# Performance work log

Hardware: AMD Instinct MI355X
Metric: run time of the kernel (lower is better)

Reference implementation:

```python
import jax, jax.numpy as jnp
import numpy as np

UP = 2


def _lpf_rect(N, cutoff):
    # ideal lowpass rect over full-FFT frequency axis (with Nyquist 0.5 fix)
    cutoff_low = int((N * cutoff) // 2)
    cutoff_high = int(N - cutoff_low)
    rect = np.ones(N, dtype=np.float32)
    rect[cutoff_low + 1:cutoff_high] = 0.0
    if (N * cutoff) % 2 == 0:
        rect[cutoff_low] = 0.5
        rect[cutoff_high] = 0.5
    return rect


def _recon_rect(N, cutoff):
    # reconstruction rect for zero-insertion upsampling (no Nyquist halving)
    cutoff_low = int((N * cutoff) // 2)
    cutoff_high = int(N - cutoff_low)
    rect = np.ones(N, dtype=np.float32)
    rect[cutoff_low + 1:cutoff_high] = 0.0
    return rect


def _rfft2_mask(rect_h, rect_w):
    # outer product mask on rfft2 grid: full H axis x half W axis
    half_w = rect_w.shape[0] // 2 + 1
    return jnp.asarray(rect_h[:, None] * rect_w[None, :half_w])


def setup_inputs() -> dict:
    key = jax.random.key(0)
    x = jax.random.normal(key, (32, 128, 64, 64), dtype=jnp.float32)
    # PolyAct default init_coef (buffer, non-trainable)
    coef = jnp.array([0.0169394634313126, 0.5, 0.3078363963999393, 0.0],
                     dtype=jnp.float32)
    return {"x": x, "coef": coef}


def reference(x, coef):
    B, C, H, W = x.shape
    Hu, Wu = H * UP, W * UP

    # ---- UpsampleRFFT: zero-insertion then ideal reconstruction filter ----
    xu = jnp.zeros((B, C, Hu, Wu), x.dtype).at[:, :, ::UP, ::UP].set(x)
    recon_mask = _rfft2_mask(_recon_rect(Hu, 1.0 / UP), _recon_rect(Wu, 1.0 / UP))
    f = jnp.fft.rfft2(xu) * (UP * UP) * recon_mask
    xu = jnp.fft.irfft2(f, s=(Hu, Wu))

    # ---- PolyAct: calc_polynomial loops range(2, deg) with deg=3, so only
    # terms up to x^2 are used (coef[3] is never applied) ----
    y = coef[0] + coef[1] * xu + coef[2] * xu * xu

    # ---- LPF_RFFT with cutoff = 1/up ----
    lpf_mask = _rfft2_mask(_lpf_rect(Hu, 1.0 / UP), _lpf_rect(Wu, 1.0 / UP))
    y = jnp.fft.irfft2(jnp.fft.rfft2(y) * lpf_mask, s=(Hu, Wu))

    # ---- decimate back to original resolution ----
    return y[:, :, ::UP, ::UP]
```

## Files before the change

### kernel.cpp

```cpp
#include <hip/hip_runtime.h>
#include <math.h>


typedef short short8 __attribute__((ext_vector_type(8)));
typedef float f32x16 __attribute__((ext_vector_type(16)));

#define LSH 68
#define GSTR 132

__device__ __forceinline__ short f2bf(float f) {
  unsigned u = __float_as_uint(f);
  u += 0x7FFFu + ((u >> 16) & 1u);
  return (short)(u >> 16);
}
__device__ __forceinline__ unsigned pkbf(float a, float b) {
  unsigned ua = __float_as_uint(a); ua += 0x7FFFu + ((ua >> 16) & 1u);
  unsigned ub = __float_as_uint(b); ub += 0x7FFFu + ((ub >> 16) & 1u);
  return (ua >> 16) | (ub & 0xFFFF0000u);
}
__device__ __forceinline__ float bflo(unsigned u) {
  return __uint_as_float(u << 16);
}
__device__ __forceinline__ float bfhi(unsigned u) {
  return __uint_as_float(u & 0xFFFF0000u);
}
__device__ __forceinline__ short8 ldrow(const short* p) {
  union { unsigned u[4]; short8 s; } v;
  const uint2 lo = *(const uint2*)p;
  const uint2 hi = *(const uint2*)(p + 4);
  v.u[0] = lo.x; v.u[1] = lo.y; v.u[2] = hi.x; v.u[3] = hi.y;
  return v.s;
}
__device__ __forceinline__ short8 tabfrag(const short* gtab, int t, int blk,
                                          int kk, int q, int l31) {
  const int s = 64 + 16 * kk + 8 * q - l31 - 32 * blk;
  const int p = s & 3;
  return ldrow(gtab + (t * 4 + p) * GSTR + (s - p));
}

__global__ void init_tables(float* ws) {
  __shared__ float g64s[64];
  const int tid = threadIdx.x;
  if (tid < 64) {
    const int d = 2 * tid + 1;
    double s = 1.0;
    for (int k = 1; k <= 32; ++k) {
      const int qq = (k * d) & 127;
      s += 2.0 * cos(M_PI * (double)qq / 64.0);
    }
    g64s[tid] = (float)(s / 64.0);
  }
  __syncthreads();
  if (tid < 128) ws[tid] = g64s[tid & 63];
  short* gt = (short*)(ws + 128);
  for (int e = tid; e < 2 * 4 * GSTR; e += 256) {
    const int t = e / (4 * GSTR);
    const int rem = e - t * 4 * GSTR;
    const int p = rem / GSTR;
    const int m = rem - p * GSTR;
    const int li = m + p;
    const int gi = t ? ((-li) & 63) : (li & 63);
    gt[e] = f2bf(g64s[gi]);
  }
}

__global__ __launch_bounds__(256, 5) void uppolyact_kernel(
    const float* __restrict__ x, const float* __restrict__ coef,
    const float* __restrict__ ws, float* __restrict__ out) {
  __shared__ __align__(16) short bufA[64 * LSH];
  __shared__ __align__(16) short bufB[64 * LSH];
  __shared__ __align__(16) short bufC[64 * LSH];
  __shared__ __align__(16) unsigned char tabs[2624];
  __shared__ float tp[256];
  __shared__ float up[256];
  __shared__ float tvec[64], uvec[64], svec[64];
  __shared__ float lrp[128];
  __shared__ float sigv;

  const float* g2f = (const float*)tabs;
  const short* gtab = (const short*)(tabs + 512);

  const int tid = threadIdx.x;
  const int lane = tid & 63;
  const int w = tid >> 6;
  const int q = lane >> 5;
  const int l31 = lane & 31;
  const int rb = w >> 1, cb = w & 1;
  const int icol = cb * 32 + l31;
  const size_t base = (size_t)blockIdx.x * 4096;

  if (tid < 164) *(float4*)&tabs[16 * tid] = ((const float4*)ws)[tid];
  {
    const float4* xv = (const float4*)(x + base);
#pragma unroll
    for (int e = 0; e < 4; ++e) {
      const int k4 = tid + 256 * e;
      const float4 v = xv[k4];
      const int r = k4 >> 4, c = (k4 & 15) << 2;
      const unsigned d0 = pkbf(v.x, v.y), d1 = pkbf(v.z, v.w);
      *(uint2*)&bufA[r * LSH + c] = make_uint2(d0, d1);
      bufB[(c + 0) * LSH + r] = (short)d0;
      bufB[(c + 1) * LSH + r] = (short)(d0 >> 16);
      bufB[(c + 2) * LSH + r] = (short)d1;
      bufB[(c + 3) * LSH + r] = (short)(d1 >> 16);
    }
  }
  __syncthreads();

  f32x16 Rt, Lt;
#pragma unroll
  for (int r = 0; r < 16; ++r) { Rt[r] = 0.0f; Lt[r] = 0.0f; }
#pragma unroll
  for (int kk = 0; kk < 4; ++kk) {
    const short8 aR = tabfrag(gtab, 1, rb, kk, q, l31);
    const short8 bR = ldrow(&bufA[(cb * 32 + l31) * LSH + kk * 16 + q * 8]);
    Rt = __builtin_amdgcn_mfma_f32_32x32x16_bf16(aR, bR, Rt, 0, 0, 0);
    const short8 aL = ldrow(&bufB[(rb * 32 + l31) * LSH + kk * 16 + q * 8]);
    const short8 bL = tabfrag(gtab, 1, cb, kk, q, l31);
    Lt = __builtin_amdgcn_mfma_f32_32x32x16_bf16(aL, bL, Lt, 0, 0, 0);
  }
  {
    const int jj = tid & 63, pp = tid >> 6;
    float tacc = 0.0f, uacc = 0.0f;
#pragma unroll
    for (int g4 = 0; g4 < 4; ++g4) {
      const uint2 dt = *(const uint2*)&bufB[jj * LSH + 16 * pp + 4 * g4];
      tacc += bflo(dt.x) - bfhi(dt.x) + bflo(dt.y) - bfhi(dt.y);
      const uint2 du = *(const uint2*)&bufA[jj * LSH + 16 * pp + 4 * g4];
      uacc += bflo(du.x) - bfhi(du.x) + bflo(du.y) - bfhi(du.y);
    }
    tp[pp * 64 + jj] = tacc;
    up[pp * 64 + jj] = uacc;
  }
  {
    float lp = 0.0f;
#pragma unroll
    for (int r = 0; r < 16; ++r) lp += (r & 1) ? -Lt[r] : Lt[r];
    lp += __shfl_xor(lp, 32);
    if (q == 0) lrp[rb * 64 + icol] = lp;
  }
  __syncthreads();

#pragma unroll
  for (int grp = 0; grp < 4; ++grp) {
    const unsigned d0 = pkbf(Lt[4 * grp + 0], Lt[4 * grp + 1]);
    const unsigned d1 = pkbf(Lt[4 * grp + 2], Lt[4 * grp + 3]);
    *(uint2*)&bufC[icol * LSH + 4 * q + 32 * rb + 8 * grp] = make_uint2(d0, d1);
  }
  if (tid < 64) {
    tvec[tid] = tp[tid] + tp[64 + tid] + tp[128 + tid] + tp[192 + tid];
  } else if (tid < 128) {
    const int i = tid - 64;
    uvec[i] = up[i] + up[64 + i] + up[128 + i] + up[192 + i];
  }
  __syncthreads();

  f32x16 OOt;
#pragma unroll
  for (int r = 0; r < 16; ++r) OOt[r] = 0.0f;
#pragma unroll
  for (int kk = 0; kk < 4; ++kk) {
    const short8 a = tabfrag(gtab, 1, rb, kk, q, l31);
    const short8 b = ldrow(&bufC[(cb * 32 + l31) * LSH + kk * 16 + q * 8]);
    OOt = __builtin_amdgcn_mfma_f32_32x32x16_bf16(a, b, OOt, 0, 0, 0);
  }
  {
    const int jj = tid & 63, pp = tid >> 6;
    float sp = 0.0f;
#pragma unroll
    for (int mm = 0; mm < 16; ++mm) {
      const int m = 16 * pp + mm;
      sp += tvec[m] * g2f[64 + jj - m];
    }
    tp[pp * 64 + jj] = sp;
  }
  if (tid >= 192) {
    const int i = tid - 192;
    float v = (i & 1) ? -uvec[i] : uvec[i];
#pragma unroll
    for (int off = 32; off >= 1; off >>= 1) v += __shfl_xor(v, off);
    if (i == 0) sigv = v;
  }
#pragma unroll
  for (int grp = 0; grp < 4; ++grp) {
    const unsigned d0 = pkbf(OOt[4 * grp + 0] * OOt[4 * grp + 0],
                             OOt[4 * grp + 1] * OOt[4 * grp + 1]);
    const unsigned d1 = pkbf(OOt[4 * grp + 2] * OOt[4 * grp + 2],
                             OOt[4 * grp + 3] * OOt[4 * grp + 3]);
    *(uint2*)&bufA[icol * LSH + 4 * q + 32 * rb + 8 * grp] = make_uint2(d0, d1);
  }
  __syncthreads();

  if (tid < 64) {
    svec[tid] = tp[tid] + tp[64 + tid] + tp[128 + tid] + tp[192 + tid];
  }
  __syncthreads();

  const float sgi = (icol & 1) ? -1.0f : 1.0f;
  const float luv_i = lrp[icol] + lrp[64 + icol];
  f32x16 Ut;
#pragma unroll
  for (int grp = 0; grp < 4; ++grp) {
    const float4 sv = *(const float4*)&svec[4 * q + 32 * rb + 8 * grp];
    float zeo[4];
#pragma unroll
    for (int rr = 0; rr < 4; ++rr) {
      const int r = 4 * grp + rr;
      const float veo = Rt[r] + sgi * (&sv.x)[rr] * (1.0f / 64.0f);
      zeo[rr] = veo * veo;
      const float sgj = (r & 1) ? -1.0f : 1.0f;
      const float voe = Lt[r] + luv_i * sgj * (1.0f / 64.0f);
      Ut[r] = voe * voe;
    }
    *(uint2*)&bufB[icol * LSH + 4 * q + 32 * rb + 8 * grp] =
        make_uint2(pkbf(zeo[0], zeo[1]), pkbf(zeo[2], zeo[3]));
  }
#pragma unroll
  for (int kk = 0; kk < 4; ++kk) {
    const short8 aU = tabfrag(gtab, 0, rb, kk, q, l31);
    const short8 bU = ldrow(&bufA[(cb * 32 + l31) * LSH + kk * 16 + q * 8]);
    Ut = __builtin_amdgcn_mfma_f32_32x32x16_bf16(aU, bU, Ut, 0, 0, 0);
  }
#pragma unroll
  for (int r = 0; r < 16; ++r) {
    const int jrow = (r & 3) + 4 * q + 8 * (r >> 2) + 32 * rb;
    bufC[jrow * LSH + icol] = f2bf(Ut[r]);
  }
  __syncthreads();

  f32x16 Wv, Vv;
#pragma unroll
  for (int r = 0; r < 16; ++r) { Wv[r] = 0.0f; Vv[r] = 0.0f; }
#pragma unroll
  for (int kk = 0; kk < 4; ++kk) {
    const short8 aW = ldrow(&bufB[(rb * 32 + l31) * LSH + kk * 16 + q * 8]);
    const short8 bW = tabfrag(gtab, 0, cb, kk, q, l31);
    Wv = __builtin_amdgcn_mfma_f32_32x32x16_bf16(aW, bW, Wv, 0, 0, 0);
    const short8 aV = tabfrag(gtab, 0, rb, kk, q, l31);
    const short8 bV = ldrow(&bufC[(cb * 32 + l31) * LSH + kk * 16 + q * 8]);
    Vv = __builtin_amdgcn_mfma_f32_32x32x16_bf16(aV, bV, Vv, 0, 0, 0);
  }

  const float c0 = coef[0], c1 = coef[1];
  const float c2q = 0.25f * coef[2];
  const float* xb = x + base;
  float* ob = out + base;
  const int jcol = icol;
  const float sgjc = (jcol & 1) ? -1.0f : 1.0f;
  const float tj = tvec[jcol];
#pragma unroll
  for (int grp = 0; grp < 4; ++grp) {
    const float4 uv = *(const float4*)&uvec[4 * q + 32 * rb + 8 * grp];
#pragma unroll
    for (int rr = 0; rr < 4; ++rr) {
      const int r = 4 * grp + rr;
      const int irow = (r & 3) + 4 * q + 8 * (r >> 2) + 32 * rb;
      const float sgir = (r & 1) ? -1.0f : 1.0f;
      const float xg = xb[irow * 64 + jcol];
      const float vee = xg + (sgir * tj + (&uv.x)[rr] * sgjc) * (1.0f / 64.0f) +
                        sgir * sgjc * sigv * (1.0f / 4096.0f);
      ob[irow * 64 + jcol] = c0 + c1 * xg + c2q * (vee * vee + Vv[r] + Wv[r]);
    }
  }
}

extern "C" void kernel_launch(void* const* d_in, const int* in_sizes, int n_in,
                              void* d_out, int out_size, void* d_ws,
                              size_t ws_size, hipStream_t stream) {
  const float* x = (const float*)d_in[0];
  const float* coef = (const float*)d_in[1];
  float* out = (float*)d_out;
  float* ws = (float*)d_ws;
  const int channels = out_size / 4096;
  init_tables<<<dim3(1), dim3(256), 0, stream>>>(ws);
  uppolyact_kernel<<<dim3(channels), dim3(256), 0, stream>>>(x, coef, ws, out);
}
```

Before: 152.1 us.

## Swizzle transposed LDS tile, reuse LDS x, stage coalesced nontemporal output stores

XOR-swizzles the transposed bf16 copy of the input in shared memory to reduce bank conflicts on its row reads. It swaps the roles of bufA and bufB so one barrier and the svec reduction step can be removed, with the partial sums now added inline. The final x values are read from the bf16 shared-memory tile instead of being re-read from global memory. Results are staged through shared memory so the output can be written with coalesced float4 nontemporal stores. Reading x as bf16 lowers the precision of the linear term, and the staging step adds two barriers.

```diff
diff --git a/kernel.cpp b/kernel.cpp
--- a/kernel.cpp
+++ b/kernel.cpp
@@ -4,9 +4,11 @@
 
 typedef short short8 __attribute__((ext_vector_type(8)));
 typedef float f32x16 __attribute__((ext_vector_type(16)));
+typedef float f32x4 __attribute__((ext_vector_type(4)));
 
 #define LSH 68
-#define GSTR 132
+#define GSTR 136
+#define FSTR 68
 
 __device__ __forceinline__ short f2bf(float f) {
   unsigned u = __float_as_uint(f);
@@ -24,12 +26,17 @@
 __device__ __forceinline__ float bfhi(unsigned u) {
   return __uint_as_float(u & 0xFFFF0000u);
 }
-__device__ __forceinline__ short8 ldrow(const short* p) {
+__device__ __forceinline__ short8 mk8(uint2 lo, uint2 hi) {
   union { unsigned u[4]; short8 s; } v;
-  const uint2 lo = *(const uint2*)p;
-  const uint2 hi = *(const uint2*)(p + 4);
   v.u[0] = lo.x; v.u[1] = lo.y; v.u[2] = hi.x; v.u[3] = hi.y;
   return v.s;
+}
+__device__ __forceinline__ short8 ldrow(const short* p) {
+  return mk8(*(const uint2*)p, *(const uint2*)(p + 4));
+}
+__device__ __forceinline__ short8 ldrow_sw(const short* rowp, int u0, int sw) {
+  return mk8(*(const uint2*)(rowp + 4 * (u0 ^ sw)),
+             *(const uint2*)(rowp + 4 * ((u0 + 1) ^ sw)));
 }
 __device__ __forceinline__ short8 tabfrag(const short* gtab, int t, int blk,
                                           int kk, int q, int l31) {
@@ -67,13 +74,15 @@
 __global__ __launch_bounds__(256, 5) void uppolyact_kernel(
     const float* __restrict__ x, const float* __restrict__ coef,
     const float* __restrict__ ws, float* __restrict__ out) {
-  __shared__ __align__(16) short bufA[64 * LSH];
-  __shared__ __align__(16) short bufB[64 * LSH];
-  __shared__ __align__(16) short bufC[64 * LSH];
-  __shared__ __align__(16) unsigned char tabs[2624];
+  __shared__ __align__(16) unsigned char arena[3 * 64 * LSH * 2];
+  short* bufA = (short*)arena;
+  short* bufB = (short*)(arena + 64 * LSH * 2);
+  short* bufC = (short*)(arena + 2 * 64 * LSH * 2);
+  float* fOut = (float*)(arena + 64 * LSH * 2);
+  __shared__ __align__(16) unsigned char tabs[2688];
   __shared__ float tp[256];
   __shared__ float up[256];
-  __shared__ float tvec[64], uvec[64], svec[64];
+  __shared__ float tvec[64], uvec[64];
   __shared__ float lrp[128];
   __shared__ float sigv;
 
@@ -89,20 +98,21 @@
   const int icol = cb * 32 + l31;
   const size_t base = (size_t)blockIdx.x * 4096;
 
-  if (tid < 164) *(float4*)&tabs[16 * tid] = ((const float4*)ws)[tid];
+  if (tid < 168) *(float4*)&tabs[16 * tid] = ((const float4*)ws)[tid];
   {
     const float4* xv = (const float4*)(x + base);
 #pragma unroll
     for (int e = 0; e < 4; ++e) {
       const int k4 = tid + 256 * e;
       const float4 v = xv[k4];
-      const int r = k4 >> 4, c = (k4 & 15) << 2;
+      const int r = k4 >> 4, c4 = k4 & 15, c = c4 << 2;
       const unsigned d0 = pkbf(v.x, v.y), d1 = pkbf(v.z, v.w);
       *(uint2*)&bufA[r * LSH + c] = make_uint2(d0, d1);
-      bufB[(c + 0) * LSH + r] = (short)d0;
-      bufB[(c + 1) * LSH + r] = (short)(d0 >> 16);
-      bufB[(c + 2) * LSH + r] = (short)d1;
-      bufB[(c + 3) * LSH + r] = (short)(d1 >> 16);
+      const int so = 4 * ((r >> 2) ^ c4) + (r & 3);
+      bufB[(c + 0) * LSH + so] = (short)d0;
+      bufB[(c + 1) * LSH + so] = (short)(d0 >> 16);
+      bufB[(c + 2) * LSH + so] = (short)d1;
+      bufB[(c + 3) * LSH + so] = (short)(d1 >> 16);
     }
   }
   __syncthreads();
@@ -110,21 +120,27 @@
   f32x16 Rt, Lt;
 #pragma unroll
   for (int r = 0; r < 16; ++r) { Rt[r] = 0.0f; Lt[r] = 0.0f; }
-#pragma unroll
-  for (int kk = 0; kk < 4; ++kk) {
-    const short8 aR = tabfrag(gtab, 1, rb, kk, q, l31);
-    const short8 bR = ldrow(&bufA[(cb * 32 + l31) * LSH + kk * 16 + q * 8]);
-    Rt = __builtin_amdgcn_mfma_f32_32x32x16_bf16(aR, bR, Rt, 0, 0, 0);
-    const short8 aL = ldrow(&bufB[(rb * 32 + l31) * LSH + kk * 16 + q * 8]);
-    const short8 bL = tabfrag(gtab, 1, cb, kk, q, l31);
-    Lt = __builtin_amdgcn_mfma_f32_32x32x16_bf16(aL, bL, Lt, 0, 0, 0);
+  {
+    const int rowA = 32 * rb + l31;
+    const int swA = (rowA >> 2) & 15;
+    const short* rowpA = &bufB[rowA * LSH];
+#pragma unroll
+    for (int kk = 0; kk < 4; ++kk) {
+      const short8 aR = tabfrag(gtab, 1, rb, kk, q, l31);
+      const short8 bR = ldrow(&bufA[(cb * 32 + l31) * LSH + kk * 16 + q * 8]);
+      Rt = __builtin_amdgcn_mfma_f32_32x32x16_bf16(aR, bR, Rt, 0, 0, 0);
+      const short8 aL = ldrow_sw(rowpA, 4 * kk + 2 * q, swA);
+      const short8 bL = tabfrag(gtab, 1, cb, kk, q, l31);
+      Lt = __builtin_amdgcn_mfma_f32_32x32x16_bf16(aL, bL, Lt, 0, 0, 0);
+    }
   }
   {
     const int jj = tid & 63, pp = tid >> 6;
+    const int swj = (jj >> 2) & 15;
     float tacc = 0.0f, uacc = 0.0f;
 #pragma unroll
     for (int g4 = 0; g4 < 4; ++g4) {
-      const uint2 dt = *(const uint2*)&bufB[jj * LSH + 16 * pp + 4 * g4];
+      const uint2 dt = *(const uint2*)&bufB[jj * LSH + 4 * ((4 * pp + g4) ^ swj)];
       tacc += bflo(dt.x) - bfhi(dt.x) + bflo(dt.y) - bfhi(dt.y);
       const uint2 du = *(const uint2*)&bufA[jj * LSH + 16 * pp + 4 * g4];
       uacc += bflo(du.x) - bfhi(du.x) + bflo(du.y) - bfhi(du.y);
@@ -181,18 +197,22 @@
     for (int off = 32; off >= 1; off >>= 1) v += __shfl_xor(v, off);
     if (i == 0) sigv = v;
   }
+  unsigned xpk[8];
+#pragma unroll
+  for (int h = 0; h < 8; ++h) {
+    const int r0 = 2 * h;
+    const int irow = (r0 & 3) + 4 * q + 8 * (r0 >> 2) + 32 * rb;
+    const unsigned lo = (unsigned short)bufA[irow * LSH + icol];
+    const unsigned hi = (unsigned short)bufA[(irow + 1) * LSH + icol];
+    xpk[h] = lo | (hi << 16);
+  }
 #pragma unroll
   for (int grp = 0; grp < 4; ++grp) {
     const unsigned d0 = pkbf(OOt[4 * grp + 0] * OOt[4 * grp + 0],
                              OOt[4 * grp + 1] * OOt[4 * grp + 1]);
     const unsigned d1 = pkbf(OOt[4 * grp + 2] * OOt[4 * grp + 2],
                              OOt[4 * grp + 3] * OOt[4 * grp + 3]);
-    *(uint2*)&bufA[icol * LSH + 4 * q + 32 * rb + 8 * grp] = make_uint2(d0, d1);
-  }
-  __syncthreads();
-
-  if (tid < 64) {
-    svec[tid] = tp[tid] + tp[64 + tid] + tp[128 + tid] + tp[192 + tid];
+    *(uint2*)&bufB[icol * LSH + 4 * q + 32 * rb + 8 * grp] = make_uint2(d0, d1);
   }
   __syncthreads();
 
@@ -201,24 +221,29 @@
   f32x16 Ut;
 #pragma unroll
   for (int grp = 0; grp < 4; ++grp) {
-    const float4 sv = *(const float4*)&svec[4 * q + 32 * rb + 8 * grp];
+    const int idx4 = 4 * q + 32 * rb + 8 * grp;
+    const float4 s0 = *(const float4*)&tp[idx4];
+    const float4 s1 = *(const float4*)&tp[64 + idx4];
+    const float4 s2 = *(const float4*)&tp[128 + idx4];
+    const float4 s3 = *(const float4*)&tp[192 + idx4];
     float zeo[4];
 #pragma unroll
     for (int rr = 0; rr < 4; ++rr) {
       const int r = 4 * grp + rr;
-      const float veo = Rt[r] + sgi * (&sv.x)[rr] * (1.0f / 64.0f);
+      const float srv = (&s0.x)[rr] + (&s1.x)[rr] + (&s2.x)[rr] + (&s3.x)[rr];
+      const float veo = Rt[r] + sgi * srv * (1.0f / 64.0f);
       zeo[rr] = veo * veo;
       const float sgj = (r & 1) ? -1.0f : 1.0f;
       const float voe = Lt[r] + luv_i * sgj * (1.0f / 64.0f);
       Ut[r] = voe * voe;
     }
-    *(uint2*)&bufB[icol * LSH + 4 * q + 32 * rb + 8 * grp] =
+    *(uint2*)&bufA[icol * LSH + idx4] =
         make_uint2(pkbf(zeo[0], zeo[1]), pkbf(zeo[2], zeo[3]));
   }
 #pragma unroll
   for (int kk = 0; kk < 4; ++kk) {
     const short8 aU = tabfrag(gtab, 0, rb, kk, q, l31);
-    const short8 bU = ldrow(&bufA[(cb * 32 + l31) * LSH + kk * 16 + q * 8]);
+    const short8 bU = ldrow(&bufB[(cb * 32 + l31) * LSH + kk * 16 + q * 8]);
     Ut = __builtin_amdgcn_mfma_f32_32x32x16_bf16(aU, bU, Ut, 0, 0, 0);
   }
 #pragma unroll
@@ -233,33 +258,46 @@
   for (int r = 0; r < 16; ++r) { Wv[r] = 0.0f; Vv[r] = 0.0f; }
 #pragma unroll
   for (int kk = 0; kk < 4; ++kk) {
-    const short8 aW = ldrow(&bufB[(rb * 32 + l31) * LSH + kk * 16 + q * 8]);
+    const short8 aW = ldrow(&bufA[(rb * 32 + l31) * LSH + kk * 16 + q * 8]);
     const short8 bW = tabfrag(gtab, 0, cb, kk, q, l31);
     Wv = __builtin_amdgcn_mfma_f32_32x32x16_bf16(aW, bW, Wv, 0, 0, 0);
     const short8 aV = tabfrag(gtab, 0, rb, kk, q, l31);
     const short8 bV = ldrow(&bufC[(cb * 32 + l31) * LSH + kk * 16 + q * 8]);
     Vv = __builtin_amdgcn_mfma_f32_32x32x16_bf16(aV, bV, Vv, 0, 0, 0);
   }
-
   const float c0 = coef[0], c1 = coef[1];
   const float c2q = 0.25f * coef[2];
-  const float* xb = x + base;
-  float* ob = out + base;
-  const int jcol = icol;
-  const float sgjc = (jcol & 1) ? -1.0f : 1.0f;
-  const float tj = tvec[jcol];
+  const float sgjc = (icol & 1) ? -1.0f : 1.0f;
+  const float tj = tvec[icol];
 #pragma unroll
   for (int grp = 0; grp < 4; ++grp) {
     const float4 uv = *(const float4*)&uvec[4 * q + 32 * rb + 8 * grp];
 #pragma unroll
     for (int rr = 0; rr < 4; ++rr) {
       const int r = 4 * grp + rr;
-      const int irow = (r & 3) + 4 * q + 8 * (r >> 2) + 32 * rb;
       const float sgir = (r & 1) ? -1.0f : 1.0f;
-      const float xg = xb[irow * 64 + jcol];
+      const float xg = (r & 1) ? bfhi(xpk[r >> 1]) : bflo(xpk[r >> 1]);
       const float vee = xg + (sgir * tj + (&uv.x)[rr] * sgjc) * (1.0f / 64.0f) +
                         sgir * sgjc * sigv * (1.0f / 4096.0f);
-      ob[irow * 64 + jcol] = c0 + c1 * xg + c2q * (vee * vee + Vv[r] + Wv[r]);
+      Vv[r] = c0 + c1 * xg + c2q * (vee * vee + Vv[r] + Wv[r]);
+    }
+  }
+  __syncthreads();
+
+#pragma unroll
+  for (int r = 0; r < 16; ++r) {
+    const int irow = (r & 3) + 4 * q + 8 * (r >> 2) + 32 * rb;
+    fOut[irow * FSTR + icol] = Vv[r];
+  }
+  __syncthreads();
+  {
+    f32x4* ov = (f32x4*)(out + base);
+#pragma unroll
+    for (int e = 0; e < 4; ++e) {
+      const int idx4 = tid + 256 * e;
+      const int row = idx4 >> 4, col4 = (idx4 & 15) << 2;
+      const f32x4 v = *(const f32x4*)&fOut[row * FSTR + col4];
+      __builtin_nontemporal_store(v, &ov[idx4]);
     }
   }
 }
```

Measured after the change: 155.6 us. +2.3%, slower.
